# Kernel optimization log

Measured on AMD Instinct MI355X. Metric: run time of the kernel, lower is better.

## Reference

```python
import jax, jax.numpy as jnp
import numpy as np

B, S, D, H = 4, 1024, 1024, 16
DK = D // H  # 64


def setup_inputs() -> dict:
    key = jax.random.key(0)
    ks = jax.random.split(key, 12)
    scale = 0.02
    inp = {
        "query": jax.random.normal(ks[0], (B, S, D), jnp.float32),
        "key": jax.random.normal(ks[1], (B, S, D), jnp.float32),
        "value": jax.random.normal(ks[2], (B, S, D), jnp.float32),
        "mask": jax.random.randint(ks[3], (B, 1, S, S), 0, 2, jnp.int32),
        "wq": jax.random.normal(ks[4], (D, D), jnp.float32) * scale,
        "bq": jnp.zeros((D,), jnp.float32),
        "wk": jax.random.normal(ks[5], (D, D), jnp.float32) * scale,
        "bk": jnp.zeros((D,), jnp.float32),
        "wv": jax.random.normal(ks[6], (D, D), jnp.float32) * scale,
        "bv": jnp.zeros((D,), jnp.float32),
        "wo": jax.random.normal(ks[7], (D, D), jnp.float32) * scale,
        "bo": jnp.zeros((D,), jnp.float32),
    }
    return inp


def reference(query, key, value, mask, wq, bq, wk, bk, wv, bv, wo, bo):
    # Linear projections (torch Linear: x @ W.T + b)
    q = query @ wq.T + bq
    k = key @ wk.T + bk
    v = value @ wv.T + bv
    # [B,S,D] -> [B,H,S,DK]
    q = q.reshape(B, S, H, DK).transpose(0, 2, 1, 3)
    k = k.reshape(B, S, H, DK).transpose(0, 2, 1, 3)
    v = v.reshape(B, S, H, DK).transpose(0, 2, 1, 3)
    # scaled dot-product attention with mask (-1e9 where mask==0)
    scores = jnp.einsum('bhqd,bhkd->bhqk', q, k) / jnp.sqrt(jnp.float32(DK))
    scores = jnp.where(mask == 0, jnp.float32(-1e9), scores)
    attn = jax.nn.softmax(scores, axis=-1)  # dropout p=0.0 -> identity
    x = jnp.einsum('bhqk,bhkd->bhqd', attn, v)
    # [B,H,S,DK] -> [B,S,D]
    x = x.transpose(0, 2, 1, 3).reshape(B, S, D)
    return x @ wo.T + bo
```

## Files before the change

### kernel.cpp

```cpp
#include <hip/hip_runtime.h>


typedef __attribute__((ext_vector_type(8))) short short8;
typedef __attribute__((ext_vector_type(4))) float f32x4;
typedef __attribute__((ext_vector_type(4))) unsigned short u16x4;
typedef unsigned short u16;
typedef unsigned long long u64;

#define SCALE_Q 0.180336880f

__device__ __forceinline__ u16 f2bf(float f) {
    unsigned u = __float_as_uint(f);
    return (u16)((u + 0x7FFFu + ((u >> 16) & 1u)) >> 16);
}

__global__ __launch_bounds__(256) void prep(
    const float* __restrict__ q, const float* __restrict__ k,
    const float* __restrict__ v, const float* __restrict__ wq,
    const float* __restrict__ wk, const float* __restrict__ wv,
    const float* __restrict__ wo, const int* __restrict__ mask,
    u16* __restrict__ xq, u16* __restrict__ xk, u16* __restrict__ xv,
    u16* __restrict__ wqb, u16* __restrict__ wkb, u16* __restrict__ wvb,
    u16* __restrict__ wob, u64* __restrict__ bits) {
    int bid = blockIdx.x;
    if (bid < 16384) {
        const float* src; u16* dst; int i;
        if (bid < 12288) {
            int chunk = bid >> 12;
            int off = bid & 4095;
            src = (chunk == 0) ? q : ((chunk == 1) ? k : v);
            dst = (chunk == 0) ? xq : ((chunk == 1) ? xk : xv);
            i = off * 256 + threadIdx.x;
        } else {
            int wb = bid - 12288;
            int chunk = wb >> 10;
            int off = wb & 1023;
            src = (chunk == 0) ? wq : ((chunk == 1) ? wk : ((chunk == 2) ? wv : wo));
            dst = (chunk == 0) ? wqb : ((chunk == 1) ? wkb : ((chunk == 2) ? wvb : wob));
            i = off * 256 + threadIdx.x;
        }
        f32x4 val = ((const f32x4*)src)[i];
        u16x4 r;
        r.x = f2bf(val.x); r.y = f2bf(val.y); r.z = f2bf(val.z); r.w = f2bf(val.w);
        ((u16x4*)dst)[i] = r;
    } else {
        int mb = bid - 16384;
        int wid = threadIdx.x >> 6, lane = threadIdx.x & 63;
        int base = mb * 1024 + wid * 256;
        #pragma unroll
        for (int j = 0; j < 4; ++j) {
            u64 bal = __ballot(mask[base + j * 64 + lane] != 0);
            if (lane == 0) bits[(base >> 6) + j] = bal;
        }
    }
}

__device__ __forceinline__ void gemm_core_128(const u16* __restrict__ A,
                                              const u16* __restrict__ B,
                                              int m0, int n0,
                                              u16* As, u16* Bs,
                                              f32x4 acc[4][4]) {
    const int t = threadIdx.x;
    const int lane = t & 63;
    const int wid = t >> 6;
    const int l15 = lane & 15;
    const int quad = lane >> 4;
    const int wm = (wid & 1) * 64;
    const int wn = (wid >> 1) * 64;
    const int sr = t >> 3;
    const int sc = t & 7;

    for (int kt = 0; kt < 1024; kt += 64) {
        __syncthreads();
        #pragma unroll
        for (int p = 0; p < 4; ++p) {
            int r = p * 32 + sr;
            int gl = sc ^ (r & 7);
            *(short8*)&As[r * 64 + gl * 8] =
                *(const short8*)&A[(size_t)(m0 + r) * 1024 + kt + sc * 8];
            *(short8*)&Bs[r * 64 + gl * 8] =
                *(const short8*)&B[(size_t)(n0 + r) * 1024 + kt + sc * 8];
        }
        __syncthreads();
        #pragma unroll
        for (int ks = 0; ks < 2; ++ks) {
            short8 af[4], bf[4];
            #pragma unroll
            for (int i = 0; i < 4; ++i) {
                int mr = wm + i * 16 + l15;
                af[i] = *(const short8*)&As[mr * 64 + (((ks << 2) + quad) ^ (mr & 7)) * 8];
                int nr = wn + i * 16 + l15;
                bf[i] = *(const short8*)&Bs[nr * 64 + (((ks << 2) + quad) ^ (nr & 7)) * 8];
            }
            #pragma unroll
            for (int mi = 0; mi < 4; ++mi)
                #pragma unroll
                for (int ni = 0; ni < 4; ++ni)
                    acc[mi][ni] = __builtin_amdgcn_mfma_f32_16x16x32_bf16(
                        af[mi], bf[ni], acc[mi][ni], 0, 0, 0);
        }
    }
}

__global__ __launch_bounds__(256) void gemm_qkv(
    const u16* __restrict__ Aq, const u16* __restrict__ Ak, const u16* __restrict__ Av,
    const u16* __restrict__ Wq, const u16* __restrict__ Wk, const u16* __restrict__ Wv,
    const float* __restrict__ bq, const float* __restrict__ bk, const float* __restrict__ bv,
    u16* __restrict__ Qo, u16* __restrict__ Ko, u16* __restrict__ VTo) {
    __shared__ __align__(16) u16 As[128 * 64];
    __shared__ __align__(16) u16 Bs[128 * 64];
    const int bn = blockIdx.x;
    const int p = bn >> 3;
    const int n0 = (bn & 7) * 128;
    const int m0 = blockIdx.y * 128;
    const u16* A = (p == 0) ? Aq : ((p == 1) ? Ak : Av);
    const u16* W = (p == 0) ? Wq : ((p == 1) ? Wk : Wv);
    const float* bias = (p == 0) ? bq : ((p == 1) ? bk : bv);

    f32x4 acc[4][4];
    #pragma unroll
    for (int i = 0; i < 4; ++i)
        #pragma unroll
        for (int j = 0; j < 4; ++j) acc[i][j] = (f32x4){0.f, 0.f, 0.f, 0.f};

    gemm_core_128(A, W, m0, n0, As, Bs, acc);

    const int lane = threadIdx.x & 63;
    const int wid = threadIdx.x >> 6;
    const int l15 = lane & 15;
    const int quad = lane >> 4;
    const int wm = (wid & 1) * 64;
    const int wn = (wid >> 1) * 64;
    u16* dst01 = (p == 0) ? Qo : Ko;
    const float qs = (p == 0) ? SCALE_Q : 1.0f;

    #pragma unroll
    for (int mi = 0; mi < 4; ++mi) {
        #pragma unroll
        for (int ni = 0; ni < 4; ++ni) {
            int col = n0 + wn + ni * 16 + l15;
            int h = col >> 6, dk = col & 63;
            float bcol = bias[col];
            if (p < 2) {
                #pragma unroll
                for (int r = 0; r < 4; ++r) {
                    int row = m0 + wm + mi * 16 + quad * 4 + r;
                    int bb = row >> 10, s = row & 1023;
                    dst01[(size_t)((bb * 16 + h) * 1024 + s) * 64 + dk] =
                        f2bf((acc[mi][ni][r] + bcol) * qs);
                }
            } else {
                int row0 = m0 + wm + mi * 16 + quad * 4;
                int bb = row0 >> 10, s0 = row0 & 1023;
                u64 pk = 0;
                #pragma unroll
                for (int r = 0; r < 4; ++r)
                    pk |= (u64)f2bf(acc[mi][ni][r] + bcol) << (16 * r);
                *(u64*)&VTo[(size_t)((bb * 16 + h) * 64 + dk) * 1024 + s0] = pk;
            }
        }
    }
}

__global__ __launch_bounds__(256) void gemm_out(
    const u16* __restrict__ X, const u16* __restrict__ Wo,
    const float* __restrict__ bo, float* __restrict__ out) {
    __shared__ __align__(16) u16 As[64 * 64];
    __shared__ __align__(16) u16 Bs[128 * 64];
    const int n0 = blockIdx.x * 128;
    const int m0 = blockIdx.y * 64;
    const int t = threadIdx.x;
    const int lane = t & 63;
    const int wid = t >> 6;
    const int l15 = lane & 15;
    const int quad = lane >> 4;
    const int wm = (wid & 1) * 32;
    const int wn = (wid >> 1) * 64;
    const int sr = t >> 3;
    const int sc = t & 7;

    f32x4 acc[2][4];
    #pragma unroll
    for (int i = 0; i < 2; ++i)
        #pragma unroll
        for (int j = 0; j < 4; ++j) acc[i][j] = (f32x4){0.f, 0.f, 0.f, 0.f};

    for (int kt = 0; kt < 1024; kt += 64) {
        __syncthreads();
        #pragma unroll
        for (int p = 0; p < 2; ++p) {
            int r = p * 32 + sr;
            int gl = sc ^ (r & 7);
            *(short8*)&As[r * 64 + gl * 8] =
                *(const short8*)&X[(size_t)(m0 + r) * 1024 + kt + sc * 8];
        }
        #pragma unroll
        for (int p = 0; p < 4; ++p) {
            int r = p * 32 + sr;
            int gl = sc ^ (r & 7);
            *(short8*)&Bs[r * 64 + gl * 8] =
                *(const short8*)&Wo[(size_t)(n0 + r) * 1024 + kt + sc * 8];
        }
        __syncthreads();
        #pragma unroll
        for (int ks = 0; ks < 2; ++ks) {
            short8 af[2], bf[4];
            #pragma unroll
            for (int i = 0; i < 2; ++i) {
                int mr = wm + i * 16 + l15;
                af[i] = *(const short8*)&As[mr * 64 + (((ks << 2) + quad) ^ (mr & 7)) * 8];
            }
            #pragma unroll
            for (int j = 0; j < 4; ++j) {
                int nr = wn + j * 16 + l15;
                bf[j] = *(const short8*)&Bs[nr * 64 + (((ks << 2) + quad) ^ (nr & 7)) * 8];
            }
            #pragma unroll
            for (int mi = 0; mi < 2; ++mi)
                #pragma unroll
                for (int ni = 0; ni < 4; ++ni)
                    acc[mi][ni] = __builtin_amdgcn_mfma_f32_16x16x32_bf16(
                        af[mi], bf[ni], acc[mi][ni], 0, 0, 0);
        }
    }

    #pragma unroll
    for (int mi = 0; mi < 2; ++mi) {
        #pragma unroll
        for (int ni = 0; ni < 4; ++ni) {
            int col = n0 + wn + ni * 16 + l15;
            float bcol = bo[col];
            #pragma unroll
            for (int r = 0; r < 4; ++r) {
                int row = m0 + wm + mi * 16 + quad * 4 + r;
                out[(size_t)row * 1024 + col] = acc[mi][ni][r] + bcol;
            }
        }
    }
}

__global__ __launch_bounds__(256) void attn_kernel(
    const u16* __restrict__ Q, const u16* __restrict__ K, const u16* __restrict__ VT,
    const u64* __restrict__ mbits, u16* __restrict__ X) {
    __shared__ __align__(16) u16 Qs[64 * 64];
    __shared__ __align__(16) u16 Ks[64 * 64];
    __shared__ __align__(16) u16 Vs[64 * 64];
    __shared__ __align__(16) u16 Ps[4][16 * 72];

    const int qt = blockIdx.x;
    const int h = blockIdx.y;
    const int b = blockIdx.z;
    const int t = threadIdx.x;
    const int lane = t & 63;
    const int wid = t >> 6;
    const int l15 = lane & 15;
    const int quad = lane >> 4;
    const int q0 = qt * 64;
    const int sr = t >> 3;
    const int sc = t & 7;

    const size_t headoff = (size_t)(b * 16 + h) * 1024 * 64;
    const u16* Qh = Q + headoff;
    const u16* Kh = K + headoff;
    const u16* Vh = VT + headoff;

    #pragma unroll
    for (int p = 0; p < 2; ++p) {
        int r = p * 32 + sr;
        int gl = sc ^ (r & 7);
        *(short8*)&Qs[r * 64 + gl * 8] =
            *(const short8*)&Qh[(size_t)(q0 + r) * 64 + sc * 8];
    }

    f32x4 o_acc[4];
    #pragma unroll
    for (int j = 0; j < 4; ++j) o_acc[j] = (f32x4){0.f, 0.f, 0.f, 0.f};
    float lacc[4] = {0.f, 0.f, 0.f, 0.f};

    const u64* mrow = &mbits[(size_t)((b << 10) + q0 + wid * 16 + quad * 4) << 4];

    for (int kt = 0; kt < 16; ++kt) {
        const int kv0 = kt * 64;
        __syncthreads();
        #pragma unroll
        for (int p = 0; p < 2; ++p) {
            int r = p * 32 + sr;
            int gl = sc ^ (r & 7);
            *(short8*)&Ks[r * 64 + gl * 8] =
                *(const short8*)&Kh[(size_t)(kv0 + r) * 64 + sc * 8];
            *(short8*)&Vs[r * 64 + gl * 8] =
                *(const short8*)&Vh[(size_t)r * 1024 + kv0 + sc * 8];
        }
        __syncthreads();

        f32x4 sacc[4];
        #pragma unroll
        for (int j = 0; j < 4; ++j) sacc[j] = (f32x4){0.f, 0.f, 0.f, 0.f};
        #pragma unroll
        for (int ks = 0; ks < 2; ++ks) {
            int m = wid * 16 + l15;
            short8 qf = *(const short8*)&Qs[m * 64 + (((ks << 2) + quad) ^ (m & 7)) * 8];
            #pragma unroll
            for (int j = 0; j < 4; ++j) {
                int n = j * 16 + l15;
                short8 kf = *(const short8*)&Ks[n * 64 + (((ks << 2) + quad) ^ (n & 7)) * 8];
                sacc[j] = __builtin_amdgcn_mfma_f32_16x16x32_bf16(qf, kf, sacc[j], 0, 0, 0);
            }
        }

        #pragma unroll
        for (int r = 0; r < 4; ++r) {
            u64 w = mrow[(r << 4) + kt];
            #pragma unroll
            for (int ni = 0; ni < 4; ++ni) {
                float p = exp2f(sacc[ni][r]);
                p = ((w >> (ni * 16 + l15)) & 1ull) ? p : 0.f;
                lacc[r] += p;
                Ps[wid][(quad * 4 + r) * 72 + ni * 16 + l15] = f2bf(p);
            }
        }

        #pragma unroll
        for (int ks = 0; ks < 2; ++ks) {
            short8 pf = *(const short8*)&Ps[wid][l15 * 72 + ks * 32 + quad * 8];
            #pragma unroll
            for (int j = 0; j < 4; ++j) {
                int d = j * 16 + l15;
                short8 vf = *(const short8*)&Vs[d * 64 + (((ks << 2) + quad) ^ (d & 7)) * 8];
                o_acc[j] = __builtin_amdgcn_mfma_f32_16x16x32_bf16(pf, vf, o_acc[j], 0, 0, 0);
            }
        }
    }

    #pragma unroll
    for (int r = 0; r < 4; ++r) {
        float l = lacc[r];
        l += __shfl_xor(l, 1);
        l += __shfl_xor(l, 2);
        l += __shfl_xor(l, 4);
        l += __shfl_xor(l, 8);
        float inv = 1.0f / l;
        int qrow = q0 + wid * 16 + quad * 4 + r;
        #pragma unroll
        for (int ni = 0; ni < 4; ++ni) {
            X[(size_t)(b * 1024 + qrow) * 1024 + h * 64 + ni * 16 + l15] =
                f2bf(o_acc[ni][r] * inv);
        }
    }
}

extern "C" void kernel_launch(void* const* d_in, const int* in_sizes, int n_in,
                              void* d_out, int out_size, void* d_ws, size_t ws_size,
                              hipStream_t stream) {
    const float* query = (const float*)d_in[0];
    const float* key_ = (const float*)d_in[1];
    const float* value = (const float*)d_in[2];
    const int* mask = (const int*)d_in[3];
    const float* wq = (const float*)d_in[4];
    const float* bq = (const float*)d_in[5];
    const float* wk = (const float*)d_in[6];
    const float* bk = (const float*)d_in[7];
    const float* wv = (const float*)d_in[8];
    const float* bv = (const float*)d_in[9];
    const float* wo = (const float*)d_in[10];
    const float* bo = (const float*)d_in[11];
    float* out = (float*)d_out;

    char* ws = (char*)d_ws;
    const size_t XB = (size_t)4096 * 1024 * 2;
    const size_t WB = (size_t)1024 * 1024 * 2;
    u16* xq = (u16*)(ws);
    u16* xk = (u16*)(ws + XB);
    u16* xv = (u16*)(ws + 2 * XB);
    u16* wqb = (u16*)(ws + 3 * XB);
    u16* wkb = (u16*)(ws + 3 * XB + WB);
    u16* wvb = (u16*)(ws + 3 * XB + 2 * WB);
    u16* wob = (u16*)(ws + 3 * XB + 3 * WB);
    u16* Qb = (u16*)(ws + 3 * XB + 4 * WB);
    u16* Kb = (u16*)(ws + 4 * XB + 4 * WB);
    u16* VTb = (u16*)(ws + 5 * XB + 4 * WB);
    u64* bits = (u64*)(ws + 6 * XB + 4 * WB);
    u16* Xattn = xq;

    prep<<<20480, 256, 0, stream>>>(query, key_, value, wq, wk, wv, wo, mask,
                                    xq, xk, xv, wqb, wkb, wvb, wob, bits);
    gemm_qkv<<<dim3(24, 32), 256, 0, stream>>>(xq, xk, xv, wqb, wkb, wvb,
                                               bq, bk, bv, Qb, Kb, VTb);
    attn_kernel<<<dim3(16, 16, 4), 256, 0, stream>>>(Qb, Kb, VTb, bits, Xattn);
    gemm_out<<<dim3(8, 64), 256, 0, stream>>>(Xattn, wob, bo, out);
}
```

Measured before the change: 255.5 us.

## Use direct global-to-LDS loads in GEMMs and prefetch K/V in attention

Both projection GEMMs now stage A and W tiles with global_load_lds 16-byte transfers straight into shared memory, skipping the register round trip. The XOR swizzle is dropped because the direct load fixes the LDS layout, so LDS bank conflicts may return. The attention kernel keeps Q fragments in registers instead of LDS and prefetches the next K/V tile into registers while the current one is computed. It also replaces the 64-bit mask shift with 32-bit shifts.

```diff
diff --git a/kernel.cpp b/kernel.cpp
--- a/kernel.cpp
+++ b/kernel.cpp
@@ -12,6 +12,12 @@
 __device__ __forceinline__ u16 f2bf(float f) {
     unsigned u = __float_as_uint(f);
     return (u16)((u + 0x7FFFu + ((u >> 16) & 1u)) >> 16);
+}
+
+__device__ __forceinline__ void gl_lds16(const u16* g, u16* l) {
+    __builtin_amdgcn_global_load_lds(
+        (__attribute__((address_space(1))) void*)g,
+        (__attribute__((address_space(3))) void*)l, 16, 0, 0);
 }
 
 __global__ __launch_bounds__(256) void prep(
@@ -55,53 +61,6 @@
     }
 }
 
-__device__ __forceinline__ void gemm_core_128(const u16* __restrict__ A,
-                                              const u16* __restrict__ B,
-                                              int m0, int n0,
-                                              u16* As, u16* Bs,
-                                              f32x4 acc[4][4]) {
-    const int t = threadIdx.x;
-    const int lane = t & 63;
-    const int wid = t >> 6;
-    const int l15 = lane & 15;
-    const int quad = lane >> 4;
-    const int wm = (wid & 1) * 64;
-    const int wn = (wid >> 1) * 64;
-    const int sr = t >> 3;
-    const int sc = t & 7;
-
-    for (int kt = 0; kt < 1024; kt += 64) {
-        __syncthreads();
-        #pragma unroll
-        for (int p = 0; p < 4; ++p) {
-            int r = p * 32 + sr;
-            int gl = sc ^ (r & 7);
-            *(short8*)&As[r * 64 + gl * 8] =
-                *(const short8*)&A[(size_t)(m0 + r) * 1024 + kt + sc * 8];
-            *(short8*)&Bs[r * 64 + gl * 8] =
-                *(const short8*)&B[(size_t)(n0 + r) * 1024 + kt + sc * 8];
-        }
-        __syncthreads();
-        #pragma unroll
-        for (int ks = 0; ks < 2; ++ks) {
-            short8 af[4], bf[4];
-            #pragma unroll
-            for (int i = 0; i < 4; ++i) {
-                int mr = wm + i * 16 + l15;
-                af[i] = *(const short8*)&As[mr * 64 + (((ks << 2) + quad) ^ (mr & 7)) * 8];
-                int nr = wn + i * 16 + l15;
-                bf[i] = *(const short8*)&Bs[nr * 64 + (((ks << 2) + quad) ^ (nr & 7)) * 8];
-            }
-            #pragma unroll
-            for (int mi = 0; mi < 4; ++mi)
-                #pragma unroll
-                for (int ni = 0; ni < 4; ++ni)
-                    acc[mi][ni] = __builtin_amdgcn_mfma_f32_16x16x32_bf16(
-                        af[mi], bf[ni], acc[mi][ni], 0, 0, 0);
-        }
-    }
-}
-
 __global__ __launch_bounds__(256) void gemm_qkv(
     const u16* __restrict__ Aq, const u16* __restrict__ Ak, const u16* __restrict__ Av,
     const u16* __restrict__ Wq, const u16* __restrict__ Wk, const u16* __restrict__ Wv,
@@ -117,23 +76,54 @@
     const u16* W = (p == 0) ? Wq : ((p == 1) ? Wk : Wv);
     const float* bias = (p == 0) ? bq : ((p == 1) ? bk : bv);
 
-    f32x4 acc[4][4];
-    #pragma unroll
-    for (int i = 0; i < 4; ++i)
-        #pragma unroll
-        for (int j = 0; j < 4; ++j) acc[i][j] = (f32x4){0.f, 0.f, 0.f, 0.f};
-
-    gemm_core_128(A, W, m0, n0, As, Bs, acc);
-
-    const int lane = threadIdx.x & 63;
-    const int wid = threadIdx.x >> 6;
+    const int t = threadIdx.x;
+    const int lane = t & 63;
+    const int wid = t >> 6;
     const int l15 = lane & 15;
     const int quad = lane >> 4;
     const int wm = (wid & 1) * 64;
     const int wn = (wid >> 1) * 64;
+    const int r8 = lane >> 3, gr = lane & 7;
+
+    f32x4 acc[4][4];
+    #pragma unroll
+    for (int i = 0; i < 4; ++i)
+        #pragma unroll
+        for (int j = 0; j < 4; ++j) acc[i][j] = (f32x4){0.f, 0.f, 0.f, 0.f};
+
+    for (int kt = 0; kt < 1024; kt += 64) {
+        __syncthreads();
+        #pragma unroll
+        for (int c = 0; c < 8; ++c) {
+            int call = wid * 8 + c;
+            if (call < 16) {
+                int rb = call * 8;
+                gl_lds16(&A[(size_t)(m0 + rb + r8) * 1024 + kt + gr * 8], &As[rb * 64]);
+            } else {
+                int rb = (call - 16) * 8;
+                gl_lds16(&W[(size_t)(n0 + rb + r8) * 1024 + kt + gr * 8], &Bs[rb * 64]);
+            }
+        }
+        __syncthreads();
+        #pragma unroll
+        for (int ks = 0; ks < 2; ++ks) {
+            short8 af[4], bf[4];
+            #pragma unroll
+            for (int i = 0; i < 4; ++i) {
+                af[i] = *(const short8*)&As[(wm + i * 16 + l15) * 64 + ks * 32 + quad * 8];
+                bf[i] = *(const short8*)&Bs[(wn + i * 16 + l15) * 64 + ks * 32 + quad * 8];
+            }
+            #pragma unroll
+            for (int mi = 0; mi < 4; ++mi)
+                #pragma unroll
+                for (int ni = 0; ni < 4; ++ni)
+                    acc[mi][ni] = __builtin_amdgcn_mfma_f32_16x16x32_bf16(
+                        af[mi], bf[ni], acc[mi][ni], 0, 0, 0);
+        }
+    }
+
     u16* dst01 = (p == 0) ? Qo : Ko;
     const float qs = (p == 0) ? SCALE_Q : 1.0f;
-
     #pragma unroll
     for (int mi = 0; mi < 4; ++mi) {
         #pragma unroll
@@ -176,8 +166,7 @@
     const int quad = lane >> 4;
     const int wm = (wid & 1) * 32;
     const int wn = (wid >> 1) * 64;
-    const int sr = t >> 3;
-    const int sc = t & 7;
+    const int r8 = lane >> 3, gr = lane & 7;
 
     f32x4 acc[2][4];
     #pragma unroll
@@ -188,33 +177,26 @@
     for (int kt = 0; kt < 1024; kt += 64) {
         __syncthreads();
         #pragma unroll
-        for (int p = 0; p < 2; ++p) {
-            int r = p * 32 + sr;
-            int gl = sc ^ (r & 7);
-            *(short8*)&As[r * 64 + gl * 8] =
-                *(const short8*)&X[(size_t)(m0 + r) * 1024 + kt + sc * 8];
-        }
-        #pragma unroll
-        for (int p = 0; p < 4; ++p) {
-            int r = p * 32 + sr;
-            int gl = sc ^ (r & 7);
-            *(short8*)&Bs[r * 64 + gl * 8] =
-                *(const short8*)&Wo[(size_t)(n0 + r) * 1024 + kt + sc * 8];
+        for (int c = 0; c < 6; ++c) {
+            int call = wid * 6 + c;
+            if (call < 8) {
+                int rb = call * 8;
+                gl_lds16(&X[(size_t)(m0 + rb + r8) * 1024 + kt + gr * 8], &As[rb * 64]);
+            } else {
+                int rb = (call - 8) * 8;
+                gl_lds16(&Wo[(size_t)(n0 + rb + r8) * 1024 + kt + gr * 8], &Bs[rb * 64]);
+            }
         }
         __syncthreads();
         #pragma unroll
         for (int ks = 0; ks < 2; ++ks) {
             short8 af[2], bf[4];
             #pragma unroll
-            for (int i = 0; i < 2; ++i) {
-                int mr = wm + i * 16 + l15;
-                af[i] = *(const short8*)&As[mr * 64 + (((ks << 2) + quad) ^ (mr & 7)) * 8];
-            }
-            #pragma unroll
-            for (int j = 0; j < 4; ++j) {
-                int nr = wn + j * 16 + l15;
-                bf[j] = *(const short8*)&Bs[nr * 64 + (((ks << 2) + quad) ^ (nr & 7)) * 8];
-            }
+            for (int i = 0; i < 2; ++i)
+                af[i] = *(const short8*)&As[(wm + i * 16 + l15) * 64 + ks * 32 + quad * 8];
+            #pragma unroll
+            for (int j = 0; j < 4; ++j)
+                bf[j] = *(const short8*)&Bs[(wn + j * 16 + l15) * 64 + ks * 32 + quad * 8];
             #pragma unroll
             for (int mi = 0; mi < 2; ++mi)
                 #pragma unroll
@@ -242,7 +224,6 @@
 __global__ __launch_bounds__(256) void attn_kernel(
     const u16* __restrict__ Q, const u16* __restrict__ K, const u16* __restrict__ VT,
     const u64* __restrict__ mbits, u16* __restrict__ X) {
-    __shared__ __align__(16) u16 Qs[64 * 64];
     __shared__ __align__(16) u16 Ks[64 * 64];
     __shared__ __align__(16) u16 Vs[64 * 64];
     __shared__ __align__(16) u16 Ps[4][16 * 72];
@@ -264,57 +245,71 @@
     const u16* Kh = K + headoff;
     const u16* Vh = VT + headoff;
 
+    short8 qf[2];
+    #pragma unroll
+    for (int ks = 0; ks < 2; ++ks)
+        qf[ks] = *(const short8*)&Qh[(size_t)(q0 + wid * 16 + l15) * 64 + ks * 32 + quad * 8];
+
+    f32x4 o_acc[4];
+    #pragma unroll
+    for (int j = 0; j < 4; ++j) o_acc[j] = (f32x4){0.f, 0.f, 0.f, 0.f};
+    float lacc[4] = {0.f, 0.f, 0.f, 0.f};
+
+    const u64* mrow = &mbits[(size_t)((b << 10) + q0 + wid * 16 + quad * 4) << 4];
+
+    short8 kpre[2], vpre[2];
     #pragma unroll
     for (int p = 0; p < 2; ++p) {
         int r = p * 32 + sr;
-        int gl = sc ^ (r & 7);
-        *(short8*)&Qs[r * 64 + gl * 8] =
-            *(const short8*)&Qh[(size_t)(q0 + r) * 64 + sc * 8];
-    }
-
-    f32x4 o_acc[4];
-    #pragma unroll
-    for (int j = 0; j < 4; ++j) o_acc[j] = (f32x4){0.f, 0.f, 0.f, 0.f};
-    float lacc[4] = {0.f, 0.f, 0.f, 0.f};
-
-    const u64* mrow = &mbits[(size_t)((b << 10) + q0 + wid * 16 + quad * 4) << 4];
+        kpre[p] = *(const short8*)&Kh[(size_t)r * 64 + sc * 8];
+        vpre[p] = *(const short8*)&Vh[(size_t)r * 1024 + sc * 8];
+    }
 
     for (int kt = 0; kt < 16; ++kt) {
-        const int kv0 = kt * 64;
         __syncthreads();
         #pragma unroll
         for (int p = 0; p < 2; ++p) {
             int r = p * 32 + sr;
             int gl = sc ^ (r & 7);
-            *(short8*)&Ks[r * 64 + gl * 8] =
-                *(const short8*)&Kh[(size_t)(kv0 + r) * 64 + sc * 8];
-            *(short8*)&Vs[r * 64 + gl * 8] =
-                *(const short8*)&Vh[(size_t)r * 1024 + kv0 + sc * 8];
-        }
-        __syncthreads();
+            *(short8*)&Ks[r * 64 + gl * 8] = kpre[p];
+            *(short8*)&Vs[r * 64 + gl * 8] = vpre[p];
+        }
+        __syncthreads();
+
+        if (kt < 15) {
+            int kvn = (kt + 1) * 64;
+            #pragma unroll
+            for (int p = 0; p < 2; ++p) {
+                int r = p * 32 + sr;
+                kpre[p] = *(const short8*)&Kh[(size_t)(kvn + r) * 64 + sc * 8];
+                vpre[p] = *(const short8*)&Vh[(size_t)r * 1024 + kvn + sc * 8];
+            }
+        }
 
         f32x4 sacc[4];
         #pragma unroll
         for (int j = 0; j < 4; ++j) sacc[j] = (f32x4){0.f, 0.f, 0.f, 0.f};
         #pragma unroll
         for (int ks = 0; ks < 2; ++ks) {
-            int m = wid * 16 + l15;
-            short8 qf = *(const short8*)&Qs[m * 64 + (((ks << 2) + quad) ^ (m & 7)) * 8];
             #pragma unroll
             for (int j = 0; j < 4; ++j) {
                 int n = j * 16 + l15;
                 short8 kf = *(const short8*)&Ks[n * 64 + (((ks << 2) + quad) ^ (n & 7)) * 8];
-                sacc[j] = __builtin_amdgcn_mfma_f32_16x16x32_bf16(qf, kf, sacc[j], 0, 0, 0);
+                sacc[j] = __builtin_amdgcn_mfma_f32_16x16x32_bf16(qf[ks], kf, sacc[j], 0, 0, 0);
             }
         }
 
         #pragma unroll
         for (int r = 0; r < 4; ++r) {
             u64 w = mrow[(r << 4) + kt];
+            unsigned t0 = (unsigned)w >> l15;
+            unsigned t1 = (unsigned)(w >> 32) >> l15;
             #pragma unroll
             for (int ni = 0; ni < 4; ++ni) {
+                unsigned bit = ((ni & 2) ? ((ni & 1) ? (t1 >> 16) : t1)
+                                         : ((ni & 1) ? (t0 >> 16) : t0)) & 1u;
                 float p = exp2f(sacc[ni][r]);
-                p = ((w >> (ni * 16 + l15)) & 1ull) ? p : 0.f;
+                p = bit ? p : 0.f;
                 lacc[r] += p;
                 Ps[wid][(quad * 4 + r) * 72 + ni * 16 + l15] = f2bf(p);
             }
```

After: 260.8 us. 1.02x slower.
